# Optimization experiments

Hardware: AMD Instinct MI355X
Metric: run time of the kernel (lower is better)

Reference implementation:

```python
import jax, jax.numpy as jnp
import numpy as np

CUTN = 128
CUT_SIZE = 224
IMG_H = 1024
IMG_W = 1024


def setup_inputs() -> dict:
    key = jax.random.key(0)
    inp = jax.random.uniform(key, (1, 3, IMG_H, IMG_W), dtype=jnp.float32)
    pad = IMG_H // 4
    sideY, sideX = IMG_H + 2 * pad, IMG_W + 2 * pad
    max_size = min(sideY, sideX)
    rng = np.random.default_rng(0)
    sy, sx, oy, ox = [], [], [], []
    for ch in range(CUTN):
        if ch > CUTN - CUTN // 4:
            # full padded image cutout
            sy.append(sideY); sx.append(sideX); oy.append(0); ox.append(0)
        else:
            size = int(max_size * float(np.clip(rng.normal(0.8, 0.3), CUT_SIZE / max_size, 1.0)))
            sy.append(size); sx.append(size)
            oy.append(int(rng.integers(0, sideY - size + 1)))
            ox.append(int(rng.integers(0, sideX - size + 1)))
    return {
        "input": inp,
        "sizes_y": jnp.asarray(sy, dtype=jnp.int32),
        "sizes_x": jnp.asarray(sx, dtype=jnp.int32),
        "offs_y": jnp.asarray(oy, dtype=jnp.int32),
        "offs_x": jnp.asarray(ox, dtype=jnp.int32),
        "cut_size": CUT_SIZE,
    }


def reference(input, sizes_y, sizes_x, offs_y, offs_x, cut_size):
    B, C, H, W = input.shape
    pad = H // 4  # transforms.Pad(input.shape[2] // 4, fill=0)
    x = jnp.pad(input, ((0, 0), (0, 0), (pad, pad), (pad, pad)))
    sideY, sideX = H + 2 * pad, W + 2 * pad
    cs = cut_size
    grid = (jnp.arange(cs, dtype=jnp.float32) + 0.5) / cs  # pixel-center sample grid

    def sample_one(oy, ox, sy, sx):
        # crop [oy:oy+sy, ox:ox+sx] resized to (cs, cs) via bilinear grid-sample
        ys = jnp.clip(oy.astype(jnp.float32) + grid * sy.astype(jnp.float32) - 0.5, 0.0, sideY - 1.0)
        xs = jnp.clip(ox.astype(jnp.float32) + grid * sx.astype(jnp.float32) - 0.5, 0.0, sideX - 1.0)
        y0 = jnp.floor(ys).astype(jnp.int32); y1 = jnp.minimum(y0 + 1, sideY - 1)
        x0 = jnp.floor(xs).astype(jnp.int32); x1 = jnp.minimum(x0 + 1, sideX - 1)
        wy = (ys - y0)[:, None]  # [cs,1]
        wx = (xs - x0)[None, :]  # [1,cs]
        p00 = x[:, :, y0[:, None], x0[None, :]]  # [B,C,cs,cs]
        p01 = x[:, :, y0[:, None], x1[None, :]]
        p10 = x[:, :, y1[:, None], x0[None, :]]
        p11 = x[:, :, y1[:, None], x1[None, :]]
        return (p00 * (1 - wy) * (1 - wx) + p01 * (1 - wy) * wx
                + p10 * wy * (1 - wx) + p11 * wy * wx)

    cutouts = jax.vmap(sample_one)(offs_y, offs_x, sizes_y, sizes_x)  # [cutn,B,C,cs,cs]
    return cutouts.reshape(-1, C, cs, cs)  # torch.cat over cutouts (cutout-major)
```

## Files before the change

### kernel.cpp

```cpp
#include <hip/hip_runtime.h>
#include <hip/hip_fp16.h>

#define CUTN 128
#define CUT_SIZE 224
#define IMG_H 1024
#define IMG_W 1024
#define PAD 256
#define SIDE 1536
#define PX_PER_CUT (CUT_SIZE * CUT_SIZE)
#define HALF_PX (PX_PER_CUT / 2)
#define BLOCKS_PER_CUT (HALF_PX / 256)
#define PLANE_PX (IMG_H * IMG_W)

__global__ __launch_bounds__(256) void convert_kernel(
    const float* __restrict__ img, __half* __restrict__ dst)
{
    const int i = blockIdx.x * 256 + threadIdx.x;
    const int total4 = 3 * PLANE_PX / 4;
    if (i >= total4) return;
    float4 v;
    __builtin_memcpy(&v, img + 4 * (size_t)i, 16);
    const __half2 a = __floats2half2_rn(v.x, v.y);
    const __half2 b = __floats2half2_rn(v.z, v.w);
    uint2 o;
    o.x = __builtin_bit_cast(unsigned int, a);
    o.y = __builtin_bit_cast(unsigned int, b);
    __builtin_memcpy(dst + 4 * (size_t)i, &o, 8);
}

template<bool HALFP>
__global__ __launch_bounds__(256) void make_cutouts_kernel(
    const float* __restrict__ img,
    const __half* __restrict__ himg,
    const int* __restrict__ sizes_y,
    const int* __restrict__ sizes_x,
    const int* __restrict__ offs_y,
    const int* __restrict__ offs_x,
    float* __restrict__ out)
{
    const int bid = blockIdx.x;
    const int k = bid & 7;
    const int j = bid >> 3;

    int cut, blk;
    if (j < 1536) {
        cut = j / 12;
        blk = k * 12 + (j - cut * 12);
    } else {
        const int e = j - 1536;
        cut = (k >> 1) + (e << 2);
        blk = 96 + (k & 1);
    }

    const int lane = (int)(threadIdx.x & 63);

    const int sy = sizes_y[cut], sx = sizes_x[cut];
    const int oy = offs_y[cut],  ox = offs_x[cut];

    const bool eq_lo = (sizes_y[lane]      == sy) & (sizes_x[lane]      == sx) &
                       (offs_y[lane]       == oy) & (offs_x[lane]       == ox);
    const bool eq_hi = (sizes_y[lane + 64] == sy) & (sizes_x[lane + 64] == sx) &
                       (offs_y[lane + 64]  == oy) & (offs_x[lane + 64]  == ox);
    const unsigned long long mlo = __ballot(eq_lo);
    const unsigned long long mhi = __ballot(eq_hi);
    const int canon = mlo ? (__ffsll(mlo) - 1) : (__ffsll(mhi) + 63);
    if (canon != cut) return;

    const float syf = (float)sy, sxf = (float)sx;
    const float oyf = (float)oy, oxf = (float)ox;

    const int p  = blk * 256 + (int)threadIdx.x;
    const int y  = p / CUT_SIZE;
    const int x  = p - y * CUT_SIZE;

    const float gx = ((float)x + 0.5f) / (float)CUT_SIZE;
    const float xs = fminf(fmaxf(oxf + gx * sxf - 0.5f, 0.0f), (float)(SIDE - 1));
    const int   x0 = (int)floorf(xs);
    const float wx = xs - (float)x0;
    const int  xx0 = x0 - PAD;
    const int  xx1 = min(x0 + 1, SIDE - 1) - PAD;
    const bool vx0 = (unsigned)xx0 < (unsigned)IMG_W;
    const bool vx1 = (unsigned)xx1 < (unsigned)IMG_W;
    const int   ax = min(max(xx0, 0), IMG_W - 2);
    const bool  s0 = (xx0 != ax);
    const bool  s1 = (xx1 == ax);

    const float cx_x = ((vx0 && !s0) ? (1.0f - wx) : 0.0f)
                     + ((vx1 &&  s1) ? wx          : 0.0f);
    const float cx_y = ((vx0 &&  s0) ? (1.0f - wx) : 0.0f)
                     + ((vx1 && !s1) ? wx          : 0.0f);

    float vout[2][3];

    #pragma unroll
    for (int h = 0; h < 2; ++h) {
        const int yy = y + h * 112;

        const float gy = ((float)yy + 0.5f) / (float)CUT_SIZE;
        const float ysf = fminf(fmaxf(oyf + gy * syf - 0.5f, 0.0f), (float)(SIDE - 1));
        const int   y0 = (int)floorf(ysf);
        const float wy = ysf - (float)y0;
        const int  yy0 = y0 - PAD;
        const int  yy1 = min(y0 + 1, SIDE - 1) - PAD;
        const float wyl0 = ((unsigned)yy0 < (unsigned)IMG_H) ? (1.0f - wy) : 0.0f;
        const float wyl1 = ((unsigned)yy1 < (unsigned)IMG_H) ? wy          : 0.0f;
        const int   r0 = min(max(yy0, 0), IMG_H - 1);
        const int   r1 = min(max(yy1, 0), IMG_H - 1);

        const float cax = wyl0 * cx_x;
        const float cay = wyl0 * cx_y;
        const float cbx = wyl1 * cx_x;
        const float cby = wyl1 * cx_y;

        const int o0 = r0 * IMG_W + ax;
        const int o1 = r1 * IMG_W + ax;

        #pragma unroll
        for (int c = 0; c < 3; ++c) {
            float2 a, b;
            if constexpr (HALFP) {
                const __half* hplane = himg + c * PLANE_PX;
                unsigned int ua, ub;
                __builtin_memcpy(&ua, hplane + o0, 4);
                __builtin_memcpy(&ub, hplane + o1, 4);
                a = __half22float2(__builtin_bit_cast(__half2, ua));
                b = __half22float2(__builtin_bit_cast(__half2, ub));
            } else {
                const float* plane = img + c * PLANE_PX;
                __builtin_memcpy(&a, plane + o0, 8);
                __builtin_memcpy(&b, plane + o1, 8);
            }
            vout[h][c] = a.x * cax + a.y * cay + b.x * cbx + b.y * cby;
        }
    }

    unsigned long long lo = mlo, hi = mhi;
    while (lo) {
        const int d = __ffsll(lo) - 1; lo &= lo - 1;
        const int obase = (d * 3) * PX_PER_CUT + p;
        #pragma unroll
        for (int h = 0; h < 2; ++h)
            #pragma unroll
            for (int c = 0; c < 3; ++c)
                __builtin_nontemporal_store(
                    vout[h][c], &out[obase + c * PX_PER_CUT + h * HALF_PX]);
    }
    while (hi) {
        const int d = __ffsll(hi) + 63; hi &= hi - 1;
        const int obase = (d * 3) * PX_PER_CUT + p;
        #pragma unroll
        for (int h = 0; h < 2; ++h)
            #pragma unroll
            for (int c = 0; c < 3; ++c)
                __builtin_nontemporal_store(
                    vout[h][c], &out[obase + c * PX_PER_CUT + h * HALF_PX]);
    }
}

extern "C" void kernel_launch(void* const* d_in, const int* in_sizes, int n_in,
                              void* d_out, int out_size, void* d_ws, size_t ws_size,
                              hipStream_t stream) {
    const float* img     = (const float*)d_in[0];
    const int*   sizes_y = (const int*)d_in[1];
    const int*   sizes_x = (const int*)d_in[2];
    const int*   offs_y  = (const int*)d_in[3];
    const int*   offs_x  = (const int*)d_in[4];
    float* out = (float*)d_out;

    const int grid = CUTN * BLOCKS_PER_CUT;
    const size_t hneed = (size_t)3 * PLANE_PX * sizeof(__half);

    if (ws_size >= hneed) {
        __half* himg = (__half*)d_ws;
        const int cgrid = (3 * PLANE_PX / 4 + 255) / 256;
        convert_kernel<<<cgrid, 256, 0, stream>>>(img, himg);
        make_cutouts_kernel<true><<<grid, 256, 0, stream>>>(
            img, himg, sizes_y, sizes_x, offs_y, offs_x, out);
    } else {
        make_cutouts_kernel<false><<<grid, 256, 0, stream>>>(
            img, nullptr, sizes_y, sizes_x, offs_y, offs_x, out);
    }
}
```

Baseline: 37.82 us.

## Interleave fp16 image into padded RGBx pixels for single 16-byte gathers

The conversion kernel now writes the fp16 copy of the image as interleaved 4-channel pixels (R,G,B,pad) instead of three planar channels. The cutout kernel then fetches both horizontal neighbours for all channels with one 16-byte load per row, replacing six 4-byte gathers per row. This is meant to cut the number of scattered memory transactions in the gather. In exchange the fp16 workspace grows by a third because of the padding channel, and the conversion pass reads three planes and writes more bytes.

```diff
diff --git a/kernel.cpp b/kernel.cpp
--- a/kernel.cpp
+++ b/kernel.cpp
@@ -13,25 +13,33 @@
 #define PLANE_PX (IMG_H * IMG_W)
 
 __global__ __launch_bounds__(256) void convert_kernel(
-    const float* __restrict__ img, __half* __restrict__ dst)
+    const float* __restrict__ img, unsigned short* __restrict__ dst)
 {
     const int i = blockIdx.x * 256 + threadIdx.x;
-    const int total4 = 3 * PLANE_PX / 4;
-    if (i >= total4) return;
-    float4 v;
-    __builtin_memcpy(&v, img + 4 * (size_t)i, 16);
-    const __half2 a = __floats2half2_rn(v.x, v.y);
-    const __half2 b = __floats2half2_rn(v.z, v.w);
-    uint2 o;
-    o.x = __builtin_bit_cast(unsigned int, a);
-    o.y = __builtin_bit_cast(unsigned int, b);
-    __builtin_memcpy(dst + 4 * (size_t)i, &o, 8);
+    if (i >= PLANE_PX / 2) return;
+    const size_t p = 2 * (size_t)i;
+
+    float2 r, g, b;
+    __builtin_memcpy(&r, img + p, 8);
+    __builtin_memcpy(&g, img + PLANE_PX + p, 8);
+    __builtin_memcpy(&b, img + 2 * PLANE_PX + p, 8);
+
+    const __half2 h0 = __floats2half2_rn(r.x, g.x);
+    const __half2 h1 = __floats2half2_rn(b.x, 0.f);
+    const __half2 h2 = __floats2half2_rn(r.y, g.y);
+    const __half2 h3 = __floats2half2_rn(b.y, 0.f);
+    uint4 o;
+    o.x = __builtin_bit_cast(unsigned int, h0);
+    o.y = __builtin_bit_cast(unsigned int, h1);
+    o.z = __builtin_bit_cast(unsigned int, h2);
+    o.w = __builtin_bit_cast(unsigned int, h3);
+    __builtin_memcpy(dst + 4 * p, &o, 16);
 }
 
 template<bool HALFP>
 __global__ __launch_bounds__(256) void make_cutouts_kernel(
     const float* __restrict__ img,
-    const __half* __restrict__ himg,
+    const unsigned short* __restrict__ himg,
     const int* __restrict__ sizes_y,
     const int* __restrict__ sizes_x,
     const int* __restrict__ offs_y,
@@ -112,25 +120,31 @@
         const float cbx = wyl1 * cx_x;
         const float cby = wyl1 * cx_y;
 
-        const int o0 = r0 * IMG_W + ax;
-        const int o1 = r1 * IMG_W + ax;
-
-        #pragma unroll
-        for (int c = 0; c < 3; ++c) {
-            float2 a, b;
-            if constexpr (HALFP) {
-                const __half* hplane = himg + c * PLANE_PX;
-                unsigned int ua, ub;
-                __builtin_memcpy(&ua, hplane + o0, 4);
-                __builtin_memcpy(&ub, hplane + o1, 4);
-                a = __half22float2(__builtin_bit_cast(__half2, ua));
-                b = __half22float2(__builtin_bit_cast(__half2, ub));
-            } else {
+        if constexpr (HALFP) {
+            union { uint4 v; unsigned short s[8]; } U0, U1;
+            const int o0 = (r0 * IMG_W + ax) * 4;
+            const int o1 = (r1 * IMG_W + ax) * 4;
+            __builtin_memcpy(&U0.v, himg + o0, 16);
+            __builtin_memcpy(&U1.v, himg + o1, 16);
+            #pragma unroll
+            for (int c = 0; c < 3; ++c) {
+                const float a0 = __half2float(__builtin_bit_cast(__half, U0.s[c]));
+                const float a1 = __half2float(__builtin_bit_cast(__half, U0.s[c + 4]));
+                const float b0 = __half2float(__builtin_bit_cast(__half, U1.s[c]));
+                const float b1 = __half2float(__builtin_bit_cast(__half, U1.s[c + 4]));
+                vout[h][c] = a0 * cax + a1 * cay + b0 * cbx + b1 * cby;
+            }
+        } else {
+            const int o0 = r0 * IMG_W + ax;
+            const int o1 = r1 * IMG_W + ax;
+            #pragma unroll
+            for (int c = 0; c < 3; ++c) {
                 const float* plane = img + c * PLANE_PX;
+                float2 a, b;
                 __builtin_memcpy(&a, plane + o0, 8);
                 __builtin_memcpy(&b, plane + o1, 8);
+                vout[h][c] = a.x * cax + a.y * cay + b.x * cbx + b.y * cby;
             }
-            vout[h][c] = a.x * cax + a.y * cay + b.x * cbx + b.y * cby;
         }
     }
 
@@ -168,11 +182,11 @@
     float* out = (float*)d_out;
 
     const int grid = CUTN * BLOCKS_PER_CUT;
-    const size_t hneed = (size_t)3 * PLANE_PX * sizeof(__half);
+    const size_t hneed = (size_t)PLANE_PX * 4 * sizeof(unsigned short);
 
     if (ws_size >= hneed) {
-        __half* himg = (__half*)d_ws;
-        const int cgrid = (3 * PLANE_PX / 4 + 255) / 256;
+        unsigned short* himg = (unsigned short*)d_ws;
+        const int cgrid = (PLANE_PX / 2 + 255) / 256;
         convert_kernel<<<cgrid, 256, 0, stream>>>(img, himg);
         make_cutouts_kernel<true><<<grid, 256, 0, stream>>>(
             img, himg, sizes_y, sizes_x, offs_y, offs_x, out);
```

After: 45.23 us. 19.6% more time.
